# Performance work log

Measured on AMD Instinct MI355X. Metric: run time of the kernel, lower is better.

## Reference

```python
import jax, jax.numpy as jnp
import numpy as np

N, F, HD, E, K, T, IDX = 50000, 128, 256, 800000, 3, 7, 0


def setup_inputs() -> dict:
    key = jax.random.key(0)
    ks = jax.random.split(key, 18)
    s = 0.05  # param init scale
    return {
        "x": jax.random.normal(ks[0], (N, F), jnp.float32),
        "edge_index": jax.random.randint(ks[1], (2, E), 0, N),
        "edge_weight": jax.random.uniform(ks[2], (E,), jnp.float32),
        "h": jax.random.normal(ks[3], (N, HD), jnp.float32),
        "c": jax.random.normal(ks[4], (N, HD), jnp.float32),
        # 4 ChebConvs on X and 4 on H (gates i, f, c, o), each with K Chebyshev weights
        "theta_x": jax.random.normal(ks[5], (4, K, F, HD), jnp.float32) * s,
        "bias_x": jnp.zeros((4, HD), jnp.float32),
        "theta_h": jax.random.normal(ks[6], (4, K, HD, HD), jnp.float32) * s,
        "bias_h": jnp.zeros((4, HD), jnp.float32),
        "w_c": jax.random.normal(ks[7], (3, HD), jnp.float32) * s,  # peephole w_c_i, w_c_f, w_c_o
        "b_gate": jnp.zeros((4, HD), jnp.float32),  # b_i, b_f, b_c, b_o
        # decoder LSTM (input_size=1, hidden=HD), torch gate order i, f, g, o
        "w_ih": jax.random.normal(ks[8], (4 * HD, 1), jnp.float32) * s,
        "w_hh": jax.random.normal(ks[9], (4 * HD, HD), jnp.float32) * s,
        "b_ih": jnp.zeros((4 * HD,), jnp.float32),
        "b_hh": jnp.zeros((4 * HD,), jnp.float32),
        "w_out": jax.random.normal(ks[10], (1, HD), jnp.float32) * s,
        "b_out": jnp.zeros((1,), jnp.float32),
    }


def _cheb_stack(feat, src, dst, w_norm):
    """Stacked Chebyshev bases [K, N, d]; L_hat = -A_norm (sym norm, lambda_max=2)."""
    def lhat(v):
        msg = w_norm[:, None] * v[src]              # [E, d] gather
        return -jax.ops.segment_sum(msg, dst, num_segments=N)  # scatter-add
    Tx = [feat]
    if K > 1:
        Tx.append(lhat(feat))
    for _ in range(2, K):
        Tx.append(2.0 * lhat(Tx[-1]) - Tx[-2])
    return jnp.stack(Tx)


def reference(x, edge_index, edge_weight, h, c, theta_x, bias_x, theta_h, bias_h,
              w_c, b_gate, w_ih, w_hh, b_ih, b_hh, w_out, b_out):
    src, dst = edge_index[0], edge_index[1]
    # ChebConv.__norm__: remove self loops, sym-normalized Laplacian, scale by 2/lambda_max=1,
    # add -I -> L_hat off-diag = -w_norm, diag = 0
    w = jnp.where(src == dst, 0.0, edge_weight)
    deg = jax.ops.segment_sum(w, src, num_segments=N)
    dis = jnp.where(deg > 0, jax.lax.rsqrt(jnp.maximum(deg, 1e-20)), 0.0)
    w_norm = dis[src] * w * dis[dst]

    # GConvLSTM encode: one conv per gate on X and on H; bases shared across gates
    gx = jnp.einsum('knf,gkfo->gno', _cheb_stack(x, src, dst, w_norm), theta_x) + bias_x[:, None, :]
    gh = jnp.einsum('knf,gkfo->gno', _cheb_stack(h, src, dst, w_norm), theta_h) + bias_h[:, None, :]
    g = gx + gh  # [4, N, HD] gates i, f, c, o
    I = jax.nn.sigmoid(g[0] + w_c[0] * c + b_gate[0])
    Fg = jax.nn.sigmoid(g[1] + w_c[1] * c + b_gate[1])
    Cn = Fg * c + I * jnp.tanh(g[2] + b_gate[2])
    O = jax.nn.sigmoid(g[3] + w_c[2] * Cn + b_gate[3])
    Hn = O * jnp.tanh(Cn)

    h0 = Hn[IDX:IDX + 1]          # [1, HD]
    c0 = Cn[IDX:IDX + 1]
    inp0 = x[IDX, -1:][None]      # [1, 1]

    def step(carry, _):
        hd, cd, inp = carry
        gates = inp @ w_ih.T + hd @ w_hh.T + b_ih + b_hh  # [1, 4*HD]
        i, f, gg, o = jnp.split(gates, 4, axis=1)
        cn = jax.nn.sigmoid(f) * cd + jax.nn.sigmoid(i) * jnp.tanh(gg)
        hn = jax.nn.sigmoid(o) * jnp.tanh(cn)
        out = hn @ w_out.T + b_out                         # [1, 1]
        return (hn, cn, out), out

    _, outs = jax.lax.scan(step, (h0, c0, inp0), None, length=T)  # [T, 1, 1]
    prediction = outs[:, :, 0]  # squeeze dim 2 -> [T, 1]
    return prediction
```

## Files before the change

kernel.cpp:

```cpp
#include <hip/hip_runtime.h>
#include <math.h>

#define NN 50000
#define FD 128
#define HDIM 256
#define NE 800000
#define NBR_CAP 512
#define M_CAP 8192
#define TT 7
#define TPB 256
#define GB 96
#define PSLICE 12
#define GRP 21
#define ECHUNK 2048
#define SB 32
#define SPIN_CAP 50000000

#define O_NBRCNT   0
#define O_MCNT     64
#define O_HSYNC    128
#define O_DEG      16512
#define O_BITMAP   216512
#define O_ZERO_END 222784
#define O_NBRNODE  222784
#define O_NBRW     224832
#define O_MS       226880
#define O_MD       259648
#define O_MW       292416
#define O_GPART    325184

__device__ __forceinline__ float sigm(float v) { return 1.f / (1.f + expf(-v)); }
__device__ __forceinline__ float dis_of(float dg) {
    return dg > 0.f ? rsqrtf(fmaxf(dg, 1e-20f)) : 0.f;
}

__global__ void k_nbr(const int* __restrict__ ei, const float* __restrict__ ew,
                      char* __restrict__ ws) {
    int*   nbrCnt = (int*)(ws + O_NBRCNT);
    int*   nbrNode= (int*)(ws + O_NBRNODE);
    float* nbrW   = (float*)(ws + O_NBRW);

    int gid = blockIdx.x * blockDim.x + threadIdx.x;
    if (gid < (O_ZERO_END - O_MCNT) / 4) ((unsigned*)(ws + O_MCNT))[gid] = 0u;

    int e0 = gid * 4;
    if (e0 >= NE) return;
    int4 d4 = *(const int4*)&ei[NE + e0];
    float4 w4 = *(const float4*)&ew[e0];
    int dd[4] = {d4.x, d4.y, d4.z, d4.w};
    float wv[4] = {w4.x, w4.y, w4.z, w4.w};
    #pragma unroll
    for (int k = 0; k < 4; ++k) {
        if (dd[k] == 0 && wv[k] != 0.f) {
            int s = ei[e0 + k];
            if (s != 0) {
                int slot = atomicAdd(nbrCnt, 1);
                if (slot < NBR_CAP) { nbrNode[slot] = s; nbrW[slot] = wv[k]; }
            }
        }
    }
}

__global__ void k_match(const int* __restrict__ ei, const float* __restrict__ ew,
                        char* __restrict__ ws) {
    const int* nbrCnt = (const int*)(ws + O_NBRCNT);
    const int* nbrNode= (const int*)(ws + O_NBRNODE);
    int*      mCnt   = (int*)(ws + O_MCNT);
    int*      mS     = (int*)(ws + O_MS);
    int*      mD     = (int*)(ws + O_MD);
    float*    mW     = (float*)(ws + O_MW);
    unsigned* bitmap = (unsigned*)(ws + O_BITMAP);

    __shared__ int sNode[NBR_CAP];
    __shared__ int sCnt;
    if (threadIdx.x == 0) sCnt = min(*nbrCnt, NBR_CAP);
    __syncthreads();
    int cnt = sCnt;
    for (int i = threadIdx.x; i < cnt; i += blockDim.x) sNode[i] = nbrNode[i];
    __syncthreads();
    if (blockIdx.x == 0 && threadIdx.x == 0) atomicOr(&bitmap[0], 1u);

    int i = blockIdx.x * blockDim.x + threadIdx.x;
    int e0 = i * 4;
    if (e0 >= NE) return;
    int4 s4 = *(const int4*)&ei[e0];
    int4 d4 = *(const int4*)&ei[NE + e0];
    float4 w4 = *(const float4*)&ew[e0];
    int ss[4] = {s4.x, s4.y, s4.z, s4.w};
    int dd[4] = {d4.x, d4.y, d4.z, d4.w};
    float wv[4] = {w4.x, w4.y, w4.z, w4.w};
    bool m[4];
    #pragma unroll
    for (int k = 0; k < 4; ++k) m[k] = (dd[k] == 0);
    for (int j = 0; j < cnt; ++j) {
        int nv = sNode[j];
        #pragma unroll
        for (int k = 0; k < 4; ++k) m[k] |= (dd[k] == nv);
    }
    #pragma unroll
    for (int k = 0; k < 4; ++k) {
        int s = ss[k], d = dd[k];
        float w = wv[k];
        if (s == d || w == 0.f || !m[k]) continue;
        int slot = atomicAdd(mCnt, 1);
        if (slot < M_CAP) { mS[slot] = s; mD[slot] = d; mW[slot] = w; }
        atomicOr(&bitmap[s >> 5], 1u << (s & 31));
        atomicOr(&bitmap[d >> 5], 1u << (d & 31));
    }
}

__global__ void k_deg(const int* __restrict__ ei, const float* __restrict__ ew,
                      char* __restrict__ ws) {
    const unsigned* bitmap = (const unsigned*)(ws + O_BITMAP);
    float* deg = (float*)(ws + O_DEG);
    int i = blockIdx.x * blockDim.x + threadIdx.x;
    int e0 = i * 4;
    if (e0 >= NE) return;
    int4 s4 = *(const int4*)&ei[e0];
    int4 d4 = *(const int4*)&ei[NE + e0];
    float4 w4 = *(const float4*)&ew[e0];
    int ss[4] = {s4.x, s4.y, s4.z, s4.w};
    int dd[4] = {d4.x, d4.y, d4.z, d4.w};
    float wv[4] = {w4.x, w4.y, w4.z, w4.w};
    #pragma unroll
    for (int k = 0; k < 4; ++k) {
        int s = ss[k];
        if (s == dd[k] || wv[k] == 0.f) continue;
        if (bitmap[s >> 5] & (1u << (s & 31)))
            atomicAdd(&deg[s], wv[k]);
    }
}

__global__ __launch_bounds__(TPB) void k_graph(
    const float* __restrict__ x, const float* __restrict__ h,
    const float* __restrict__ theta_x, const float* __restrict__ theta_h,
    char* __restrict__ ws) {

    const float* deg    = (const float*)(ws + O_DEG);
    const int*   nbrCnt = (const int*)(ws + O_NBRCNT);
    const int*   mCnt   = (const int*)(ws + O_MCNT);
    const int*   nbrNode= (const int*)(ws + O_NBRNODE);
    const float* nbrW   = (const float*)(ws + O_NBRW);
    const int*   mS     = (const int*)(ws + O_MS);
    const int*   mD     = (const int*)(ws + O_MD);
    const float* mW     = (const float*)(ws + O_MW);
    float*       gpart  = (float*)(ws + O_GPART);

    __shared__ int   sNode[NBR_CAP];
    __shared__ float sWl[NBR_CAP];
    __shared__ float cf1[ECHUNK], cf2[ECHUNK];
    __shared__ int   sS[ECHUNK];
    __shared__ float tp1[GRP][PSLICE], tp2[GRP][PSLICE];
    __shared__ float tslice[PSLICE];
    __shared__ int   sCnt, sMcnt;

    const int tid = threadIdx.x, bid = blockIdx.x;
    if (tid == 0) { sCnt = min(*nbrCnt, NBR_CAP); sMcnt = min(*mCnt, M_CAP); }
    __syncthreads();
    const int ncnt = sCnt, mcnt = sMcnt;
    for (int i = tid; i < ncnt; i += TPB) { sNode[i] = nbrNode[i]; sWl[i] = nbrW[i]; }
    __syncthreads();

    const bool isx = bid < 32;
    const int qstart = bid * PSLICE - (isx ? 0 : 3 * FD);
    const float* fb0 = isx ? x : h;
    const int fstride = isx ? FD : HDIM;

    const int pl = tid % PSLICE, gr = tid / PSLICE;
    const float* fbase = fb0 + (qstart + pl) % fstride;
    const float dis0 = dis_of(deg[0]);

    float a1 = 0.f, a2 = 0.f;
    for (int c0i = 0; c0i < mcnt; c0i += ECHUNK) {
        int clen = min(ECHUNK, mcnt - c0i);
        for (int i = tid; i < clen; i += TPB) {
            int sI = mS[c0i + i], dI = mD[c0i + i];
            float w = mW[c0i + i];
            float disd = dis_of(deg[dI]);
            float wn = dis_of(deg[sI]) * w * disd;
            float Wd = 0.f;
            for (int j = 0; j < ncnt; ++j) Wd += (sNode[j] == dI) ? sWl[j] : 0.f;
            cf1[i] = (dI == 0) ? wn : 0.f;
            cf2[i] = wn * (dis0 * disd * Wd);
            sS[i] = sI;
        }
        __syncthreads();
        if (gr < GRP) {
            int i = gr;
            for (; i + 3 * GRP < clen; i += 4 * GRP) {
                int s0 = sS[i], s1 = sS[i + GRP], s2 = sS[i + 2 * GRP], s3 = sS[i + 3 * GRP];
                float c10 = cf1[i], c11 = cf1[i + GRP], c12 = cf1[i + 2 * GRP], c13 = cf1[i + 3 * GRP];
                float c20 = cf2[i], c21 = cf2[i + GRP], c22 = cf2[i + 2 * GRP], c23 = cf2[i + 3 * GRP];
                float v0 = fbase[(size_t)s0 * fstride];
                float v1 = fbase[(size_t)s1 * fstride];
                float v2 = fbase[(size_t)s2 * fstride];
                float v3 = fbase[(size_t)s3 * fstride];
                a1 += c10 * v0 + c11 * v1 + c12 * v2 + c13 * v3;
                a2 += c20 * v0 + c21 * v1 + c22 * v2 + c23 * v3;
            }
            for (; i < clen; i += GRP) {
                float v = fbase[(size_t)sS[i] * fstride];
                a1 += cf1[i] * v;
                a2 += cf2[i] * v;
            }
        }
        __syncthreads();
    }
    if (gr < GRP) { tp1[gr][pl] = a1; tp2[gr][pl] = a2; }
    __syncthreads();
    if (tid < PSLICE) {
        float A1 = 0.f, A2 = 0.f;
        #pragma unroll
        for (int g2 = 0; g2 < GRP; ++g2) { A1 += tp1[g2][tid]; A2 += tp2[g2][tid]; }
        int q = qstart + tid;
        int ko = q / fstride;
        float ff0 = fb0[q % fstride];
        tslice[tid] = (ko == 0) ? ff0 : ((ko == 1) ? -A1 : 2.f * A2 - ff0);
    }
    __syncthreads();

    {
        const float* tb = isx ? theta_x : theta_h;
        const size_t gs = isx ? (size_t)(3 * FD) * HDIM : (size_t)(3 * HDIM) * HDIM;
        float g0 = 0.f, g1 = 0.f, g2v = 0.f, g3 = 0.f;
        #pragma unroll
        for (int pp = 0; pp < PSLICE; ++pp) {
            float tv = tslice[pp];
            const float* row = tb + (size_t)(qstart + pp) * HDIM;
            g0  += tv * row[tid];
            g1  += tv * row[gs + tid];
            g2v += tv * row[2 * gs + tid];
            g3  += tv * row[3 * gs + tid];
        }
        float* gp = gpart + (size_t)bid * 1024;
        gp[tid] = g0;
        gp[HDIM + tid] = g1;
        gp[2 * HDIM + tid] = g2v;
        gp[3 * HDIM + tid] = g3;
    }
}

__global__ __launch_bounds__(TPB) void k_tail2(
    const float* __restrict__ x, const float* __restrict__ c,
    const float* __restrict__ bias_x, const float* __restrict__ bias_h,
    const float* __restrict__ w_c, const float* __restrict__ b_gate,
    const float* __restrict__ w_ih, const float* __restrict__ w_hh,
    const float* __restrict__ b_ih, const float* __restrict__ b_hh,
    const float* __restrict__ w_out, const float* __restrict__ b_out,
    float* __restrict__ out, char* __restrict__ ws) {

    unsigned long long* hsync = (unsigned long long*)(ws + O_HSYNC);
    const float* gpart = (const float*)(ws + O_GPART);

    __shared__ __align__(16) float sh[HDIM];
    __shared__ float sdot[32];
    __shared__ float swsum[4];

    const int tid = threadIdx.x, bid = blockIdx.x;

    const int rl = tid >> 3, seg = tid & 7;
    const int grow = (rl >> 3) * HDIM + bid * 8 + (rl & 7);
    float4 wreg[8];
    #pragma unroll
    for (int k = 0; k < 8; ++k)
        wreg[k] = *(const float4*)&w_hh[(size_t)grow * HDIM + seg * 32 + k * 4];
    const float wih_r = w_ih[grow];
    const float br    = b_ih[grow] + b_hh[grow];
    const float bo    = b_out[0];
    const float wout_r = w_out[tid];

    {
        const int d = tid >> 3, j = tid & 7;
        const int g = d >> 3, kk = d & 7, o = bid * 8 + kk;
        float s = 0.f;
        #pragma unroll
        for (int pb = j; pb < GB; pb += 8) s += gpart[(size_t)pb * 1024 + g * HDIM + o];
        s += __shfl_down(s, 4);
        s += __shfl_down(s, 2);
        s += __shfl_down(s, 1);
        if (j == 0) sdot[d] = s;
    }
    __syncthreads();

    float creg = 0.f;
    if (tid < 8) {
        const int o = bid * 8 + tid;
        float g0 = sdot[tid]      + bias_x[o]            + bias_h[o];
        float g1 = sdot[8 + tid]  + bias_x[HDIM + o]     + bias_h[HDIM + o];
        float g2 = sdot[16 + tid] + bias_x[2 * HDIM + o] + bias_h[2 * HDIM + o];
        float g3 = sdot[24 + tid] + bias_x[3 * HDIM + o] + bias_h[3 * HDIM + o];
        float c0 = c[o];
        float I  = sigm(g0 + w_c[o] * c0 + b_gate[o]);
        float Fg = sigm(g1 + w_c[HDIM + o] * c0 + b_gate[HDIM + o]);
        float Cn = Fg * c0 + I * tanhf(g2 + b_gate[2 * HDIM + o]);
        float O  = sigm(g3 + w_c[2 * HDIM + o] * Cn + b_gate[3 * HDIM + o]);
        float h0 = O * tanhf(Cn);
        creg = Cn;
        unsigned long long pk = (1ull << 32) | (unsigned long long)__float_as_uint(h0);
        __hip_atomic_store(&hsync[o], pk, __ATOMIC_RELAXED, __HIP_MEMORY_SCOPE_SYSTEM);
    }
    {
        unsigned long long v;
        int sp = 0;
        do {
            v = __hip_atomic_load(&hsync[tid], __ATOMIC_RELAXED, __HIP_MEMORY_SCOPE_SYSTEM);
            if ((unsigned)(v >> 32) == 1u) break;
        } while (++sp < SPIN_CAP);
        sh[tid] = __uint_as_float((unsigned)v);
    }
    __syncthreads();
    float sinp = x[FD - 1];

    for (int t = 0; t < TT; ++t) {
        float acc = 0.f;
        const float* shh = &sh[seg * 32];
        #pragma unroll
        for (int k = 0; k < 8; ++k) {
            float4 hv = *(const float4*)&shh[k * 4];
            acc += hv.x * wreg[k].x + hv.y * wreg[k].y + hv.z * wreg[k].z + hv.w * wreg[k].w;
        }
        acc += __shfl_down(acc, 4);
        acc += __shfl_down(acc, 2);
        acc += __shfl_down(acc, 1);
        if (seg == 0) sdot[rl] = acc + sinp * wih_r + br;
        __syncthreads();
        if (tid < 8) {
            float iv = sdot[tid], fv = sdot[8 + tid], gv = sdot[16 + tid], ov = sdot[24 + tid];
            float cn = sigm(fv) * creg + sigm(iv) * tanhf(gv);
            float hn = sigm(ov) * tanhf(cn);
            creg = cn;
            unsigned long long pk = (((unsigned long long)(t + 2)) << 32)
                                  | (unsigned long long)__float_as_uint(hn);
            __hip_atomic_store(&hsync[(t + 1) * HDIM + bid * 8 + tid], pk,
                               __ATOMIC_RELAXED, __HIP_MEMORY_SCOPE_SYSTEM);
        }
        float hval;
        {
            unsigned long long v;
            int sp = 0;
            do {
                v = __hip_atomic_load(&hsync[(t + 1) * HDIM + tid],
                                      __ATOMIC_RELAXED, __HIP_MEMORY_SCOPE_SYSTEM);
                if ((unsigned)(v >> 32) == (unsigned)(t + 2)) break;
            } while (++sp < SPIN_CAP);
            hval = __uint_as_float((unsigned)v);
        }
        sh[tid] = hval;
        float pw = wout_r * hval;
        pw += __shfl_down(pw, 32);
        pw += __shfl_down(pw, 16);
        pw += __shfl_down(pw, 8);
        pw += __shfl_down(pw, 4);
        pw += __shfl_down(pw, 2);
        pw += __shfl_down(pw, 1);
        if ((tid & 63) == 0) swsum[tid >> 6] = pw;
        __syncthreads();
        float sval = swsum[0] + swsum[1] + swsum[2] + swsum[3] + bo;
        sinp = sval;
        if (bid == 0 && tid == 0) out[t] = sval;
    }
}

extern "C" void kernel_launch(void* const* d_in, const int* in_sizes, int n_in,
                              void* d_out, int out_size, void* d_ws, size_t ws_size,
                              hipStream_t stream) {
    const float* x       = (const float*)d_in[0];
    const int*   ei      = (const int*)d_in[1];
    const float* ew      = (const float*)d_in[2];
    const float* h       = (const float*)d_in[3];
    const float* c       = (const float*)d_in[4];
    const float* theta_x = (const float*)d_in[5];
    const float* bias_x  = (const float*)d_in[6];
    const float* theta_h = (const float*)d_in[7];
    const float* bias_h  = (const float*)d_in[8];
    const float* w_c     = (const float*)d_in[9];
    const float* b_gate  = (const float*)d_in[10];
    const float* w_ih    = (const float*)d_in[11];
    const float* w_hh    = (const float*)d_in[12];
    const float* b_ih    = (const float*)d_in[13];
    const float* b_hh    = (const float*)d_in[14];
    const float* w_out   = (const float*)d_in[15];
    const float* b_out   = (const float*)d_in[16];
    char* ws = (char*)d_ws;
    float* out = (float*)d_out;

    hipMemsetAsync(ws, 0, 64, stream);

    int eb4 = (NE / 4 + TPB - 1) / TPB;
    k_nbr<<<eb4, TPB, 0, stream>>>(ei, ew, ws);
    k_match<<<eb4, TPB, 0, stream>>>(ei, ew, ws);
    k_deg<<<eb4, TPB, 0, stream>>>(ei, ew, ws);
    k_graph<<<GB, TPB, 0, stream>>>(x, h, theta_x, theta_h, ws);
    k_tail2<<<SB, TPB, 0, stream>>>(x, c, bias_x, bias_h, w_c, b_gate,
                                    w_ih, w_hh, b_ih, b_hh, w_out, b_out, out, ws);
}
```

Before: 52.87 us.

## Replace per-element packed hidden-state polling with per-block release/acquire flags

```diff
diff --git a/kernel.cpp b/kernel.cpp
--- a/kernel.cpp
+++ b/kernel.cpp
@@ -18,20 +18,27 @@
 
 #define O_NBRCNT   0
 #define O_MCNT     64
-#define O_HSYNC    128
-#define O_DEG      16512
-#define O_BITMAP   216512
-#define O_ZERO_END 222784
-#define O_NBRNODE  222784
-#define O_NBRW     224832
-#define O_MS       226880
-#define O_MD       259648
-#define O_MW       292416
-#define O_GPART    325184
+#define O_HFLAG    128
+#define O_HPAY     16512
+#define O_DEG      24704
+#define O_BITMAP   224704
+#define O_ZERO_END 230976
+#define O_NBRNODE  230976
+#define O_NBRW     233024
+#define O_MS       235072
+#define O_MD       267840
+#define O_MW       300608
+#define O_GPART    333376
 
 __device__ __forceinline__ float sigm(float v) { return 1.f / (1.f + expf(-v)); }
 __device__ __forceinline__ float dis_of(float dg) {
     return dg > 0.f ? rsqrtf(fmaxf(dg, 1e-20f)) : 0.f;
+}
+__device__ __forceinline__ float slf(const float* p) {
+    return __hip_atomic_load(p, __ATOMIC_RELAXED, __HIP_MEMORY_SCOPE_SYSTEM);
+}
+__device__ __forceinline__ void ssf(float* p, float v) {
+    __hip_atomic_store(p, v, __ATOMIC_RELAXED, __HIP_MEMORY_SCOPE_SYSTEM);
 }
 
 __global__ void k_nbr(const int* __restrict__ ei, const float* __restrict__ ew,
@@ -249,7 +256,8 @@
     const float* __restrict__ w_out, const float* __restrict__ b_out,
     float* __restrict__ out, char* __restrict__ ws) {
 
-    unsigned long long* hsync = (unsigned long long*)(ws + O_HSYNC);
+    unsigned* hflag = (unsigned*)(ws + O_HFLAG);
+    float*    hpay  = (float*)(ws + O_HPAY);
     const float* gpart = (const float*)(ws + O_GPART);
 
     __shared__ __align__(16) float sh[HDIM];
@@ -294,20 +302,20 @@
         float Fg = sigm(g1 + w_c[HDIM + o] * c0 + b_gate[HDIM + o]);
         float Cn = Fg * c0 + I * tanhf(g2 + b_gate[2 * HDIM + o]);
         float O  = sigm(g3 + w_c[2 * HDIM + o] * Cn + b_gate[3 * HDIM + o]);
-        float h0 = O * tanhf(Cn);
         creg = Cn;
-        unsigned long long pk = (1ull << 32) | (unsigned long long)__float_as_uint(h0);
-        __hip_atomic_store(&hsync[o], pk, __ATOMIC_RELAXED, __HIP_MEMORY_SCOPE_SYSTEM);
-    }
-    {
-        unsigned long long v;
+        ssf(&hpay[o], O * tanhf(Cn));
+    }
+    if (tid == 0)
+        __hip_atomic_store(&hflag[bid * 16], 1u, __ATOMIC_RELEASE,
+                           __HIP_MEMORY_SCOPE_SYSTEM);
+    if (tid < SB) {
         int sp = 0;
-        do {
-            v = __hip_atomic_load(&hsync[tid], __ATOMIC_RELAXED, __HIP_MEMORY_SCOPE_SYSTEM);
-            if ((unsigned)(v >> 32) == 1u) break;
-        } while (++sp < SPIN_CAP);
-        sh[tid] = __uint_as_float((unsigned)v);
-    }
+        while (__hip_atomic_load(&hflag[tid * 16], __ATOMIC_ACQUIRE,
+                                 __HIP_MEMORY_SCOPE_SYSTEM) == 0u)
+            if (++sp > SPIN_CAP) break;
+    }
+    __syncthreads();
+    sh[tid] = slf(&hpay[tid]);
     __syncthreads();
     float sinp = x[FD - 1];
 
@@ -329,22 +337,19 @@
             float cn = sigm(fv) * creg + sigm(iv) * tanhf(gv);
             float hn = sigm(ov) * tanhf(cn);
             creg = cn;
-            unsigned long long pk = (((unsigned long long)(t + 2)) << 32)
-                                  | (unsigned long long)__float_as_uint(hn);
-            __hip_atomic_store(&hsync[(t + 1) * HDIM + bid * 8 + tid], pk,
-                               __ATOMIC_RELAXED, __HIP_MEMORY_SCOPE_SYSTEM);
-        }
-        float hval;
-        {
-            unsigned long long v;
+            ssf(&hpay[(t + 1) * HDIM + bid * 8 + tid], hn);
+        }
+        if (tid == 0)
+            __hip_atomic_store(&hflag[((t + 1) * SB + bid) * 16], 1u, __ATOMIC_RELEASE,
+                               __HIP_MEMORY_SCOPE_SYSTEM);
+        if (tid < SB) {
             int sp = 0;
-            do {
-                v = __hip_atomic_load(&hsync[(t + 1) * HDIM + tid],
-                                      __ATOMIC_RELAXED, __HIP_MEMORY_SCOPE_SYSTEM);
-                if ((unsigned)(v >> 32) == (unsigned)(t + 2)) break;
-            } while (++sp < SPIN_CAP);
-            hval = __uint_as_float((unsigned)v);
-        }
+            while (__hip_atomic_load(&hflag[((t + 1) * SB + tid) * 16], __ATOMIC_ACQUIRE,
+                                     __HIP_MEMORY_SCOPE_SYSTEM) == 0u)
+                if (++sp > SPIN_CAP) break;
+        }
+        __syncthreads();
+        float hval = slf(&hpay[(t + 1) * HDIM + tid]);
         sh[tid] = hval;
         float pw = wout_r * hval;
         pw += __shfl_down(pw, 32);
```

Result: slower. 59.33 us (+12.2%).
